# Kernel tuning notes

Measured on AMD Instinct MI355X. Metric: run time of the kernel, lower is better.

Reference implementation:

```python
import jax, jax.numpy as jnp
import numpy as np

# ---- problem constants (match init_kwargs / input_specs) ----
N = 10000        # atoms
E = 160000       # edges
G = 16           # graphs in batch
Z = 10           # num_elements
K = 64           # channels (count of 0e in hidden_irreps)
NB = 8           # num_bessel
SH = 9           # (max_ell+1)^2, max_ell=2
HID = 16         # MLP_irreps 16x0e
R_MAX = 5.0
AVG_NEI = 16.0
P = 5            # num_polynomial_cutoff
L_SLICES = ((0, 1, 0), (1, 4, 1), (4, 9, 2))  # (start, end, l) per irrep block


def _sph(u):
    # real spherical harmonics, 'component' normalization, lmax=2 -> 9 comps
    x, y, z = u[:, 0], u[:, 1], u[:, 2]
    s3, s15, s5 = 3.0 ** 0.5, 15.0 ** 0.5, 5.0 ** 0.5
    one = jnp.ones_like(x)
    return jnp.stack([one,
                      s3 * x, s3 * y, s3 * z,
                      s15 * x * y, s15 * y * z,
                      0.5 * s5 * (3.0 * z * z - 1.0),
                      s15 * x * z, 0.5 * s15 * (x * x - y * y)], axis=-1)


def _radial(r):
    # Bessel basis * polynomial cutoff (p=5)
    n = jnp.arange(1, NB + 1, dtype=r.dtype)
    bess = (2.0 / R_MAX) ** 0.5 * jnp.sin(n[None, :] * jnp.pi * r[:, None] / R_MAX) / r[:, None]
    xx = r / R_MAX
    f = (1.0 - 0.5 * (P + 1) * (P + 2) * xx ** P + P * (P + 2) * xx ** (P + 1)
         - 0.5 * P * (P + 1) * xx ** (P + 2)) * (xx < 1.0)
    return bess * f[:, None]


def _total_energy(positions, node_attrs, shifts, atomic_energies, W_embed, W_up,
                  R1, R2, R3, R4, W_out, W_sc, theta, W_mix, w_read0, Wr1, Wr2,
                  edge_index, batch):
    sender, receiver = edge_index[0], edge_index[1]
    vec = positions[receiver] - positions[sender] + shifts          # [E,3]
    r = jnp.sqrt(jnp.sum(vec * vec, axis=-1) + 1e-9)                # [E]
    u = vec / r[:, None]
    sh = _sph(u)                                                     # [E,9]
    edge_feats = _radial(r)                                          # [E,NB]

    node_e0 = node_attrs @ atomic_energies                           # [N]
    energies = jax.ops.segment_sum(node_e0, batch, num_segments=G)   # [G]

    feats = node_attrs @ W_embed                                     # [N,K] scalar feats
    for i in range(2):
        h = feats @ W_up[i]                                          # [N,K]
        xw = jax.nn.silu(edge_feats @ R1[i])
        xw = jax.nn.silu(xw @ R2[i])
        xw = jax.nn.silu(xw @ R3[i])
        rw = xw @ R4[i]                                              # [E,K] TP weights
        # channel-wise tensor product message + scatter to receiver
        m = rw[:, :, None] * h[sender][:, :, None] * sh[:, None, :]  # [E,K,9]
        A = jax.ops.segment_sum(m, receiver, num_segments=N) / AVG_NEI  # [N,K,9]
        A = jnp.concatenate([jnp.einsum('nkc,kj->njc', A[:, :, s:e], W_out[i, l])
                             for (s, e, l) in L_SLICES], axis=-1)    # per-l linear
        sc = jnp.einsum('nk,nz,zkj->nj', feats, node_attrs, W_sc[i])  # residual (0e)
        # symmetric-contraction product block (correlation=3), element-dependent
        a0 = A[:, :, 0]
        w = jnp.einsum('nz,pzk->pnk', node_attrs, theta[i])           # [3,N,K]
        B = (w[0] + w[1] * a0 + w[2] * a0 * a0)[:, :, None] * A      # [N,K,9]
        B = jnp.einsum('nkc,kj->njc', B, W_mix[i])
        B = B.at[:, :, 0].add(sc)
        feats = B[:, :, 0]                                            # invariant part
        if i == 0:
            node_e = feats @ w_read0                                  # linear readout
        else:
            node_e = jax.nn.silu(feats @ Wr1) @ Wr2                   # nonlinear readout
        energies = energies + jax.ops.segment_sum(node_e, batch, num_segments=G)
    return energies                                                   # [G]


def setup_inputs() -> dict:
    key = jax.random.key(0)
    ks = jax.random.split(key, 24)
    positions = jax.random.normal(ks[0], (N, 3), jnp.float32) * 1.5
    elems = jax.random.randint(ks[1], (N,), 0, Z)
    node_attrs = jax.nn.one_hot(elems, Z, dtype=jnp.float32)
    edge_index = jax.random.randint(ks[2], (2, E), 0, N)
    batch = jnp.sort(jax.random.randint(ks[3], (N,), 0, G))
    shifts = jnp.zeros((E, 3), jnp.float32)
    rn = lambda k, sh, s: jax.random.normal(k, sh, jnp.float32) * s
    return {
        'positions': positions, 'node_attrs': node_attrs, 'shifts': shifts,
        'atomic_energies': rn(ks[4], (Z,), 1.0),
        'W_embed': rn(ks[5], (Z, K), Z ** -0.5),
        'W_up': rn(ks[6], (2, K, K), K ** -0.5),
        'R1': rn(ks[7], (2, NB, 64), NB ** -0.5),
        'R2': rn(ks[8], (2, 64, 64), 64 ** -0.5),
        'R3': rn(ks[9], (2, 64, 64), 64 ** -0.5),
        'R4': rn(ks[10], (2, 64, K), 64 ** -0.5),
        'W_out': rn(ks[11], (2, 3, K, K), K ** -0.5),
        'W_sc': rn(ks[12], (2, Z, K, K), (Z * K) ** -0.5),
        'theta': rn(ks[13], (2, 3, Z, K), 0.1),
        'W_mix': rn(ks[14], (2, K, K), K ** -0.5),
        'w_read0': rn(ks[15], (K,), K ** -0.5),
        'Wr1': rn(ks[16], (K, HID), K ** -0.5),
        'Wr2': rn(ks[17], (HID,), HID ** -0.5),
        'edge_index': edge_index, 'batch': batch,
    }


def reference(positions, node_attrs, shifts, atomic_energies, W_embed, W_up,
              R1, R2, R3, R4, W_out, W_sc, theta, W_mix, w_read0, Wr1, Wr2,
              edge_index, batch):
    def energy(pos):
        return _total_energy(pos, node_attrs, shifts, atomic_energies, W_embed, W_up,
                             R1, R2, R3, R4, W_out, W_sc, theta, W_mix,
                             w_read0, Wr1, Wr2, edge_index, batch)
    total_energy, vjp_fn = jax.vjp(energy, positions)
    (g_pos,) = vjp_fn(jnp.ones((G,), positions.dtype))
    forces = -g_pos
    return total_energy, forces
```

## Files before the change

### kernel.cpp

```cpp
#include <hip/hip_runtime.h>
#include <math.h>

#define N_NODES 10000
#define N_EDGES 160000
#define G_SEG 16
#define ZDIM 10
#define KDIM 64
#define NBESS 8
#define HIDR 16
#define RMAXF 5.0f
#define AVG_NEI_F 16.0f
#define TBINS 256
#define ZROW (TBINS+1)

__device__ __forceinline__ float siluf(float x){ float s = 1.0f/(1.0f+expf(-x)); return x*s; }
__device__ __forceinline__ float dsiluf(float x){ float s = 1.0f/(1.0f+expf(-x)); return s*(1.0f + x*(1.0f-s)); }

__device__ __forceinline__ float waveReduce(float v){
  for (int off = 32; off > 0; off >>= 1) v += __shfl_down(v, off);
  return v;
}

#define GATHER_NODE(NODE, PTR, PACK, IDXEXPR, LOADH, OUT) { \
  int beg_ = PTR[NODE]; int deg_ = PTR[(NODE)+1] - beg_; \
  float a0_=0.f,a1_=0.f,a2_=0.f,a3_=0.f; \
  for (int base_=0; base_<deg_; base_+=64){ \
    int m_ = min(64, deg_-base_); \
    int b_l = ZROW; float f_l = 0.f; int ix_l = 0; \
    if (lane < m_){ \
      int4 pk = PACK[beg_+base_+lane]; \
      float tp_ = __int_as_float(pk.x) * (TBINS/RMAXF); \
      b_l = (int)tp_; f_l = tp_ - (float)b_l; ix_l = IDXEXPR; \
    } \
    int mr_ = (m_ + 7) & ~7; \
    for (int i_=0; i_<mr_; i_+=8){ \
      int b0_=__shfl(b_l,i_),   b1_=__shfl(b_l,i_+1), b2_=__shfl(b_l,i_+2), b3_=__shfl(b_l,i_+3); \
      int b4_=__shfl(b_l,i_+4), b5_=__shfl(b_l,i_+5), b6_=__shfl(b_l,i_+6), b7_=__shfl(b_l,i_+7); \
      float f0_=__shfl(f_l,i_),   f1_=__shfl(f_l,i_+1), f2_=__shfl(f_l,i_+2), f3_=__shfl(f_l,i_+3); \
      float f4_=__shfl(f_l,i_+4), f5_=__shfl(f_l,i_+5), f6_=__shfl(f_l,i_+6), f7_=__shfl(f_l,i_+7); \
      int s0_=__shfl(ix_l,i_),   s1_=__shfl(ix_l,i_+1), s2_=__shfl(ix_l,i_+2), s3_=__shfl(ix_l,i_+3); \
      int s4_=__shfl(ix_l,i_+4), s5_=__shfl(ix_l,i_+5), s6_=__shfl(ix_l,i_+6), s7_=__shfl(ix_l,i_+7); \
      float2 F0_=Ft2[b0_*KDIM+lane]; float h0_=LOADH(s0_); \
      float2 F1_=Ft2[b1_*KDIM+lane]; float h1_=LOADH(s1_); \
      float2 F2_=Ft2[b2_*KDIM+lane]; float h2_=LOADH(s2_); \
      float2 F3_=Ft2[b3_*KDIM+lane]; float h3_=LOADH(s3_); \
      float2 F4_=Ft2[b4_*KDIM+lane]; float h4_=LOADH(s4_); \
      float2 F5_=Ft2[b5_*KDIM+lane]; float h5_=LOADH(s5_); \
      float2 F6_=Ft2[b6_*KDIM+lane]; float h6_=LOADH(s6_); \
      float2 F7_=Ft2[b7_*KDIM+lane]; float h7_=LOADH(s7_); \
      a0_ += (F0_.x + f0_*(F0_.y-F0_.x))*h0_; a1_ += (F1_.x + f1_*(F1_.y-F1_.x))*h1_; \
      a2_ += (F2_.x + f2_*(F2_.y-F2_.x))*h2_; a3_ += (F3_.x + f3_*(F3_.y-F3_.x))*h3_; \
      a0_ += (F4_.x + f4_*(F4_.y-F4_.x))*h4_; a1_ += (F5_.x + f5_*(F5_.y-F5_.x))*h5_; \
      a2_ += (F6_.x + f6_*(F6_.y-F6_.x))*h6_; a3_ += (F7_.x + f7_*(F7_.y-F7_.x))*h7_; \
    } } \
  OUT = ((a0_+a1_)+(a2_+a3_)); }

#define COOPMV(INV, W, OUTV) { \
  lds_in[w][lane] = INV; \
  __syncthreads(); \
  { float p0_=0.f,p1_=0.f,p2_=0.f,p3__=0.f; \
    const float* Wb_ = (W) + (w*16)*KDIM + lane; \
    _Pragma("unroll") \
    for (int kk_=0; kk_<16; kk_++){ \
      float wrow_ = Wb_[kk_*KDIM]; \
      int k_ = w*16 + kk_; \
      p0_  += lds_in[0][k_]*wrow_; \
      p1_  += lds_in[1][k_]*wrow_; \
      p2_  += lds_in[2][k_]*wrow_; \
      p3__ += lds_in[3][k_]*wrow_; \
    } \
    lds_part[w][0][lane]=p0_; lds_part[w][1][lane]=p1_; \
    lds_part[w][2][lane]=p2_; lds_part[w][3][lane]=p3__; } \
  __syncthreads(); \
  OUTV = ((lds_part[0][w][lane]+lds_part[1][w][lane]) + \
          (lds_part[2][w][lane]+lds_part[3][w][lane])); }

#define MV4R(V, W, OUT) { \
  float x0_=0.f,x1_=0.f,x2_=0.f,x3_=0.f; \
  for (int k_=0;k_<KDIM;k_+=4){ \
    x0_ += __shfl(V,k_)  *W[k_*KDIM+lane]; \
    x1_ += __shfl(V,k_+1)*W[(k_+1)*KDIM+lane]; \
    x2_ += __shfl(V,k_+2)*W[(k_+2)*KDIM+lane]; \
    x3_ += __shfl(V,k_+3)*W[(k_+3)*KDIM+lane]; \
  } OUT = (x0_+x1_)+(x2_+x3_); }

#define LOADH_PLAIN(S) rows[(S)*KDIM + lane]
#define LOADH_G2(S)    gAr2c[(S)*KDIM + lane].x

#define NTABW 514
#define SETUP_BASE 153
#define NSETUP (SETUP_BASE + (NTABW+3)/4)

__global__ __launch_bounds__(256) void k_setup(
    const float* We, const float* Wup, const float* Wsc,
    const float* Wout, const float* Wmix,
    const float* Wr1,
    const float* attrs, const float* aE,
    const float* R1g, const float* R2g, const float* R3g, const float* R4g,
    float* M0, float* Msc0,
    float* WoT0, float* WoT1, float* WmixT0, float* WupT1,
    float* P1, float* Qtab,
    float2* Ft2_0, float2* Ft2_1, float* dF4f,
    int* z_buf, float* e_node){
  int blk = blockIdx.x, tid = threadIdx.x;
  const float* Wmix1 = Wmix + KDIM*KDIM;
  const float* Wsc1  = Wsc + ZDIM*KDIM*KDIM;
  if (blk < 5){
    int idx = blk*256 + tid;
    if (idx < 1280){
      int which = idx >= 640;
      int t = which ? idx - 640 : idx;
      int z = t >> 6, j = t & 63;
      float acc = 0.f;
      if (!which){
        #pragma unroll 8
        for (int k = 0; k < KDIM; k++) acc += We[z*KDIM + k] * Wup[k*KDIM + j];
        M0[z*KDIM + j] = acc;
      } else {
        #pragma unroll 8
        for (int k = 0; k < KDIM; k++) acc += We[z*KDIM + k] * Wsc[(z*KDIM + k)*KDIM + j];
        Msc0[z*KDIM + j] = acc;
      }
    }
  } else if (blk < 69){
    int t = (blk-5)*256 + tid;
    int arr = t >> 12;
    int rem = t & 4095;
    int j = rem >> 6, k = rem & 63;
    float v; float* dst;
    switch(arr){
      case 0: v = Wout[k*KDIM + j];                 dst = WoT0;   break;
      case 1: v = Wout[3*KDIM*KDIM + k*KDIM + j];   dst = WoT1;   break;
      case 2: v = Wmix[k*KDIM + j];                 dst = WmixT0; break;
      default:v = Wup[KDIM*KDIM + k*KDIM + j];      dst = WupT1;  break;
    }
    dst[rem] = v;
  } else if (blk < 73){
    int t = (blk-69)*256 + tid;
    int h = t >> 6, k = t & 63;
    float acc = 0.f;
    #pragma unroll 8
    for (int j = 0; j < KDIM; j++) acc += Wr1[j*HIDR + h] * Wmix1[k*KDIM + j];
    P1[h*KDIM + k] = acc;
  } else if (blk < 113){
    int t = (blk-73)*256 + tid;
    int z = t >> 10;
    int rem = t & 1023;
    int h = rem >> 6, k = rem & 63;
    float acc = 0.f;
    #pragma unroll 8
    for (int j = 0; j < KDIM; j++) acc += Wr1[j*HIDR + h] * Wsc1[(z*KDIM + k)*KDIM + j];
    Qtab[(z*HIDR + h)*KDIM + k] = acc;
  } else if (blk < SETUP_BASE){
    int n = (blk-113)*256 + tid;
    if (n < N_NODES){
      int z = 0;
      for (int i = 1; i < ZDIM; i++) if (attrs[n*ZDIM+i] > 0.5f) z = i;
      z_buf[n] = z;
      e_node[n] = aE[z];
    }
  } else {
    int w = tid >> 6, j = tid & 63;
    int wave_id = (blk - SETUP_BASE)*4 + w;
    if (wave_id >= NTABW) return;
    int i = wave_id / (TBINS+1);
    int t = wave_id % (TBINS+1);
    float efv = 0.f, defv = 0.f;
    {
      double r = (double)t * (double)RMAXF / (double)TBINS;
      double wfr = (double)(j+1) * M_PI / (double)RMAXF;
      double c = sqrt(2.0 / (double)RMAXF);
      double bess, dbess;
      if (r < 1e-12){ bess = c*wfr; dbess = 0.0; }
      else {
        double sw = sin(wfr*r), cw = cos(wfr*r);
        bess = c*sw/r;
        dbess = c*(wfr*cw*r - sw)/(r*r);
      }
      double xx = r / (double)RMAXF;
      double f = 0.0, df = 0.0;
      if (xx < 1.0){
        double x2 = xx*xx, x4 = x2*x2, x5 = x4*xx, x6 = x5*xx, x7 = x6*xx;
        f = 1.0 - 21.0*x5 + 35.0*x6 - 15.0*x7;
        df = (-105.0*x4 + 210.0*x5 - 105.0*x6) / (double)RMAXF;
      }
      efv  = (float)(bess*f);
      defv = (float)(dbess*f + bess*df);
    }
    const float* R1 = R1g + i*NBESS*KDIM;
    const float* R2 = R2g + i*KDIM*KDIM;
    const float* R3 = R3g + i*KDIM*KDIM;
    const float* R4 = R4g + i*KDIM*KDIM;
    float z = 0.f, dz = 0.f;
    #pragma unroll
    for (int b = 0; b < NBESS; b++){
      float ef = __shfl(efv, b), def = __shfl(defv, b);
      float wv = R1[b*KDIM+j];
      z += ef*wv; dz += def*wv;
    }
    float v = siluf(z), dv = dsiluf(z)*dz;
    z = 0.f; dz = 0.f;
    for (int k = 0; k < KDIM; k++){
      float xv = __shfl(v, k), dxv = __shfl(dv, k);
      float wv = R2[k*KDIM+j];
      z += xv*wv; dz += dxv*wv;
    }
    float v2 = siluf(z), dv2 = dsiluf(z)*dz;
    z = 0.f; dz = 0.f;
    for (int k = 0; k < KDIM; k++){
      float xv = __shfl(v2, k), dxv = __shfl(dv2, k);
      float wv = R3[k*KDIM+j];
      z += xv*wv; dz += dxv*wv;
    }
    float v3 = siluf(z), dv3 = dsiluf(z)*dz;
    z = 0.f; dz = 0.f;
    for (int k = 0; k < KDIM; k++){
      float xv = __shfl(v3, k), dxv = __shfl(dv3, k);
      float wv = R4[k*KDIM+j];
      z += xv*wv; dz += dxv*wv;
    }
    float2* Ft = i ? Ft2_1 : Ft2_0;
    Ft[t*KDIM+j].x = z;  if (t > 0) Ft[(t-1)*KDIM+j].y = z;
    dF4f[(t*KDIM+j)*4 + 2*i] = dz;
    if (t > 0) dF4f[((t-1)*KDIM+j)*4 + 2*i + 1] = dz;
    if (t == 0) Ft[ZROW*KDIM + j] = make_float2(0.f, 0.f);
  }
}

__global__ __launch_bounds__(256) void k_edge_setup(const float* pos, const float* shifts, const int* ei,
                                                    const int* z_buf,
                                                    float4* evec, int4* emeta,
                                                    int* cnt_r, int* cnt_s){
  int e = blockIdx.x*256 + threadIdx.x;
  int s = ei[e], rcv = ei[N_EDGES + e];
  float dx = pos[rcv*3+0] - pos[s*3+0] + shifts[e*3+0];
  float dy = pos[rcv*3+1] - pos[s*3+1] + shifts[e*3+1];
  float dz = pos[rcv*3+2] - pos[s*3+2] + shifts[e*3+2];
  float r = sqrtf(dx*dx + dy*dy + dz*dz + 1e-9f);
  evec[e] = make_float4(dx, dy, dz, r);
  emeta[e] = make_int4(__float_as_int(r), s, rcv, z_buf[s]);
  if (r < RMAXF){
    atomicAdd(&cnt_s[s], 1);
    atomicAdd(&cnt_r[rcv], 1);
  }
}

__global__ __launch_bounds__(1024) void k_scan(const int* cnt_r, int* ptr_r, int* cur_r,
                                               const int* cnt_s, int* ptr_s, int* cur_s){
  __shared__ int wtot[16];
  __shared__ int woff[16];
  int tid = threadIdx.x;
  int w = tid >> 6, lane = tid & 63;
  const int* cnt = blockIdx.x ? cnt_s : cnt_r;
  int* ptr = blockIdx.x ? ptr_s : ptr_r;
  int* cur = blockIdx.x ? cur_s : cur_r;
  const int per = 10;
  int start = tid*per;
  int csum = 0;
  int cl[per];
  #pragma unroll
  for (int t = 0; t < per; t++){
    int i = start + t;
    int c = (i < N_NODES) ? cnt[i] : 0;
    cl[t] = c; csum += c;
  }
  int v = csum;
  #pragma unroll
  for (int off = 1; off < 64; off <<= 1){
    int u = __shfl_up(v, off);
    if (lane >= off) v += u;
  }
  if (lane == 63) wtot[w] = v;
  __syncthreads();
  if (w == 0 && lane < 16){
    int t = wtot[lane];
    int sv = t;
    #pragma unroll
    for (int off = 1; off < 16; off <<= 1){
      int u = __shfl_up(sv, off);
      if (lane >= off) sv += u;
    }
    woff[lane] = sv - t;
    if (lane == 15) ptr[N_NODES] = sv;
  }
  __syncthreads();
  int run = woff[w] + v - csum;
  #pragma unroll
  for (int t = 0; t < per; t++){
    int i = start + t;
    if (i < N_NODES){ ptr[i] = run; cur[i] = run; run += cl[t]; }
  }
}

__global__ __launch_bounds__(256) void k_fill(const int4* emeta, int* cur_r, int* cur_s,
                                              int4* pr_pack, int4* ps_pack){
  int e = blockIdx.x*256 + threadIdx.x;
  int4 m = emeta[e];
  float r = __int_as_float(m.x);
  if (r >= RMAXF) return;
  int p = atomicAdd(&cur_s[m.y], 1);
  ps_pack[p] = make_int4(m.x, m.z, e, 0);
  int p2 = atomicAdd(&cur_r[m.z], 1);
  pr_pack[p2] = make_int4(m.x, m.y, m.w, e);
}

__global__ __launch_bounds__(256) void k_layer0_fwd(
    const int* z_buf, const int* ptr_r, const int4* pr_pack,
    const float2* Ft2, const float* M0,
    const float* Wout0, const float* theta0, const float* Wmix0,
    const float* Msc0, const float* w_read0,
    const float* Wup1, const float* Wsc1,
    float* A0_out, float* h1, float* sc1, float* e_node){
  __shared__ float lds_in[4][KDIM];
  __shared__ float lds_part[4][4][KDIM];
  int tid = threadIdx.x;
  int w = tid >> 6, lane = tid & 63;
  int node = blockIdx.x*4 + w;
  int z = z_buf[node];
  const float* rows = M0;
  float acc;
  GATHER_NODE(node, ptr_r, pr_pack, pk.z, LOADH_PLAIN, acc)
  acc *= (1.0f/AVG_NEI_F);
  float a0;
  COOPMV(acc, Wout0, a0)
  A0_out[node*KDIM+lane] = a0;
  float t0 = theta0[(0*ZDIM+z)*KDIM+lane];
  float t1 = theta0[(1*ZDIM+z)*KDIM+lane];
  float t2 = theta0[(2*ZDIM+z)*KDIM+lane];
  float v = (t0 + t1*a0 + t2*a0*a0)*a0;
  float f;
  COOPMV(v, Wmix0, f)
  f += Msc0[z*KDIM+lane];
  float p = waveReduce(f * w_read0[lane]);
  if (lane == 0) e_node[node] += p;
  float h;
  COOPMV(f, Wup1, h)
  h1[node*KDIM+lane] = h;
  const float* Wz = Wsc1 + z*KDIM*KDIM;
  float s;
  MV4R(f, Wz, s)
  sc1[node*KDIM+lane] = s;
}

__global__ __launch_bounds__(256) void k_layer1_fwd_bwd(
    const int* z_buf, const int* ptr_r, const int4* pr_pack,
    const float2* Ft2, const float* h1,
    const float* Wout1, const float* theta1, const float* Wmix1,
    const float* sc1, const float* Wr1, const float* Wr2,
    const float* P1, const float* Qtab, const float* WoT1, const float* w_read0,
    float2* gAr2, float* gF1, float* e_node){
  __shared__ float lds_in[4][KDIM];
  __shared__ float lds_part[4][4][KDIM];
  int tid = threadIdx.x;
  int w = tid >> 6, lane = tid & 63;
  int node = blockIdx.x*4 + w;
  int z = z_buf[node];
  const float* rows = h1;
  float acc;
  GATHER_NODE(node, ptr_r, pr_pack, pk.y, LOADH_PLAIN, acc)
  acc *= (1.0f/AVG_NEI_F);
  float a0;
  COOPMV(acc, Wout1, a0)
  float t0 = theta1[(0*ZDIM+z)*KDIM+lane];
  float t1 = theta1[(1*ZDIM+z)*KDIM+lane];
  float t2 = theta1[(2*ZDIM+z)*KDIM+lane];
  float v = (t0 + t1*a0 + t2*a0*a0)*a0;
  float f;
  COOPMV(v, Wmix1, f)
  f += sc1[node*KDIM+lane];
  int hh = lane & 15;
  float tp0 = 0.f, tp1 = 0.f;
  for (int j = 0; j < KDIM; j += 2){
    tp0 += __shfl(f,j)  *Wr1[j*HIDR+hh];
    tp1 += __shfl(f,j+1)*Wr1[(j+1)*HIDR+hh];
  }
  float tpart = tp0 + tp1;
  float wr2 = Wr2[hh];
  float ne = waveReduce(siluf(tpart)*wr2);
  if (lane == 0) e_node[node] += 0.25f*ne;
  float coeff = dsiluf(tpart)*wr2;
  float gP0=0.f, gP1=0.f, gs0=0.f, gs1=0.f;
  const float* Qz = Qtab + z*HIDR*KDIM;
  #pragma unroll
  for (int h2 = 0; h2 < HIDR; h2 += 2){
    float c0 = __shfl(coeff, h2), c1 = __shfl(coeff, h2+1);
    gP0 += c0*P1[h2*KDIM+lane];
    gP1 += c1*P1[(h2+1)*KDIM+lane];
    gs0 += c0*Qz[h2*KDIM+lane];
    gs1 += c1*Qz[(h2+1)*KDIM+lane];
  }
  gF1[node*KDIM+lane] = w_read0[lane] + gs0 + gs1;
  float u = t0 + 2.f*t1*a0 + 3.f*t2*a0*a0;
  float vl = (gP0+gP1)*u;
  float gAr;
  COOPMV(vl, WoT1, gAr)
  gAr2[node*KDIM+lane].x = gAr * (1.0f/AVG_NEI_F);
}

__global__ __launch_bounds__(256) void k_energy(const float* e_node, const int* batch, float* out_e){
  __shared__ float part[G_SEG];
  int tid = threadIdx.x;
  if (tid < G_SEG) part[tid] = 0.f;
  __syncthreads();
  int n = blockIdx.x*256 + tid;
  if (n < N_NODES) atomicAdd(&part[batch[n]], e_node[n]);
  __syncthreads();
  if (tid < G_SEG) atomicAdd(&out_e[tid], part[tid]);
}

__global__ __launch_bounds__(256) void k_bwd_gH0(
    const int* z_buf, const int* ptr_s, const int4* ps_pack,
    const float2* Ft2, const float2* gAr2c, const float* WupT1, const float* gF1,
    const float* A00, const float* WmixT0, const float* WoT0, const float* theta0,
    float2* gAr2){
  __shared__ float lds_in[4][KDIM];
  __shared__ float lds_part[4][4][KDIM];
  int tid = threadIdx.x;
  int w = tid >> 6, lane = tid & 63;
  int node = blockIdx.x*4 + w;
  float ga;
  GATHER_NODE(node, ptr_s, ps_pack, pk.y, LOADH_G2, ga)
  float gfh;
  COOPMV(ga, WupT1, gfh)
  float gt = gF1[node*KDIM+lane] + gfh;
  float gP;
  COOPMV(gt, WmixT0, gP)
  int z = z_buf[node];
  float a = A00[node*KDIM+lane];
  float t0 = theta0[(0*ZDIM+z)*KDIM+lane];
  float t1 = theta0[(1*ZDIM+z)*KDIM+lane];
  float t2 = theta0[(2*ZDIM+z)*KDIM+lane];
  float u = t0 + 2.f*t1*a + 3.f*t2*a*a;
  float vl = gP*u;
  float gAr;
  COOPMV(vl, WoT0, gAr)
  gAr2[node*KDIM+lane].y = gAr * (1.0f/AVG_NEI_F);
}

__global__ __launch_bounds__(256) void k_gr(const int4* emeta, const float4* dF4,
                                            const float2* gAr2, const float* h1, const float* M0,
                                            float4* evec){
  int tid = threadIdx.x;
  int w = tid>>6, lane = tid&63;
  int e = blockIdx.x*4 + w;
  int4 m = emeta[e];
  float r = __int_as_float(m.x);
  if (r >= RMAXF) return;
  float tp = r * (TBINS / RMAXF);
  int b = (int)tp; if (b > TBINS-1) b = TBINS-1;
  float fr = tp - (float)b;
  float4 d4 = dF4[b*KDIM + lane];
  float2 g  = gAr2[m.z*KDIM + lane];
  float hv1 = h1[m.y*KDIM + lane];
  float hv0 = M0[m.w*KDIM + lane];
  float v = g.x*hv1*(d4.z + fr*(d4.w - d4.z)) + g.y*hv0*(d4.x + fr*(d4.y - d4.x));
  v = waveReduce(v);
  if (lane == 0) evec[e].w = v / r;
}

__global__ __launch_bounds__(256) void k_force(const int* ptr_r, const int4* pr_pack,
                                               const int* ptr_s, const int4* ps_pack,
                                               const float4* evec,
                                               float* out_f){
  int tid = threadIdx.x;
  int node = blockIdx.x*16 + (tid >> 4);
  int li = tid & 15;
  float fx=0.f, fy=0.f, fz=0.f;
  int beg = ptr_r[node], end = ptr_r[node+1];
  for (int idx = beg + li; idx < end; idx += 16){
    int e = pr_pack[idx].w;
    float4 ev = evec[e];
    fx -= ev.w*ev.x; fy -= ev.w*ev.y; fz -= ev.w*ev.z;
  }
  beg = ptr_s[node]; end = ptr_s[node+1];
  for (int idx = beg + li; idx < end; idx += 16){
    int e = ps_pack[idx].z;
    float4 ev = evec[e];
    fx += ev.w*ev.x; fy += ev.w*ev.y; fz += ev.w*ev.z;
  }
  #pragma unroll
  for (int off = 8; off > 0; off >>= 1){
    fx += __shfl_xor(fx, off);
    fy += __shfl_xor(fy, off);
    fz += __shfl_xor(fz, off);
  }
  if (li == 0){
    out_f[node*3+0] = fx; out_f[node*3+1] = fy; out_f[node*3+2] = fz;
  }
}

extern "C" void kernel_launch(void* const* d_in, const int* in_sizes, int n_in,
                              void* d_out, int out_size, void* d_ws, size_t ws_size,
                              hipStream_t stream){
  const float* pos    = (const float*)d_in[0];
  const float* attrs  = (const float*)d_in[1];
  const float* shifts = (const float*)d_in[2];
  const float* aE     = (const float*)d_in[3];
  const float* We     = (const float*)d_in[4];
  const float* Wup    = (const float*)d_in[5];
  const float* R1     = (const float*)d_in[6];
  const float* R2     = (const float*)d_in[7];
  const float* R3     = (const float*)d_in[8];
  const float* R4     = (const float*)d_in[9];
  const float* Wout   = (const float*)d_in[10];
  const float* Wsc    = (const float*)d_in[11];
  const float* theta  = (const float*)d_in[12];
  const float* Wmix   = (const float*)d_in[13];
  const float* w_read0= (const float*)d_in[14];
  const float* Wr1    = (const float*)d_in[15];
  const float* Wr2    = (const float*)d_in[16];
  const int*   ei     = (const int*)d_in[17];
  const int*   batch  = (const int*)d_in[18];

  char* base = (char*)d_ws;
  size_t off = 0;
  auto alloc = [&](size_t bytes)->void*{
    void* p = base + off;
    off = (off + bytes + 255) & ~(size_t)255;
    return p;
  };
  float4* evec   = (float4*)alloc(N_EDGES*sizeof(float4));
  int4*   emeta  = (int4*)alloc(N_EDGES*sizeof(int4));
  int4*   pr_pack= (int4*)alloc(N_EDGES*sizeof(int4));
  int4*   ps_pack= (int4*)alloc(N_EDGES*sizeof(int4));
  float*  e_node = (float*)alloc(N_NODES*sizeof(float));
  float*  h1     = (float*)alloc(N_NODES*KDIM*sizeof(float));
  float*  sc1    = (float*)alloc(N_NODES*KDIM*sizeof(float));
  float*  A00    = (float*)alloc(N_NODES*KDIM*sizeof(float));
  float*  gF1    = (float*)alloc(N_NODES*KDIM*sizeof(float));
  float2* gAr2   = (float2*)alloc(N_NODES*KDIM*sizeof(float2));
  float2* Ft2_0  = (float2*)alloc((TBINS+2)*KDIM*sizeof(float2));
  float2* Ft2_1  = (float2*)alloc((TBINS+2)*KDIM*sizeof(float2));
  float4* dF4    = (float4*)alloc((TBINS+1)*KDIM*sizeof(float4));
  float*  M0     = (float*)alloc(ZDIM*KDIM*sizeof(float));
  float*  Msc0   = (float*)alloc(ZDIM*KDIM*sizeof(float));
  float*  WoT0   = (float*)alloc(KDIM*KDIM*sizeof(float));
  float*  WoT1   = (float*)alloc(KDIM*KDIM*sizeof(float));
  float*  WmixT0 = (float*)alloc(KDIM*KDIM*sizeof(float));
  float*  WupT1  = (float*)alloc(KDIM*KDIM*sizeof(float));
  float*  P1     = (float*)alloc(HIDR*KDIM*sizeof(float));
  float*  Qtab   = (float*)alloc(ZDIM*HIDR*KDIM*sizeof(float));
  int* z_buf = (int*)alloc(N_NODES*sizeof(int));
  int* cnt_r = (int*)alloc(N_NODES*sizeof(int));
  int* cnt_s = (int*)alloc(N_NODES*sizeof(int));
  int* ptr_r = (int*)alloc((N_NODES+1)*sizeof(int));
  int* ptr_s = (int*)alloc((N_NODES+1)*sizeof(int));
  int* cur_r = (int*)alloc(N_NODES*sizeof(int));
  int* cur_s = (int*)alloc(N_NODES*sizeof(int));

  float* out_e = (float*)d_out;
  float* out_f = out_e + G_SEG;

  hipMemsetAsync(d_out, 0, (size_t)out_size*sizeof(float), stream);
  hipMemsetAsync(cnt_r, 0, N_NODES*sizeof(int), stream);
  hipMemsetAsync(cnt_s, 0, N_NODES*sizeof(int), stream);

  const int NB4 = N_NODES/4;
  const int EB  = N_EDGES/256;
  const int EB4 = N_EDGES/4;
  const int NBt = (N_NODES+255)/256;

  const float* Wup1 = Wup + KDIM*KDIM;
  const float* Wsc1 = Wsc + ZDIM*KDIM*KDIM;
  const float* Wout1 = Wout + 3*KDIM*KDIM;
  const float* theta1 = theta + 3*ZDIM*KDIM;
  const float* Wmix1 = Wmix + KDIM*KDIM;

  k_setup<<<NSETUP,256,0,stream>>>(We, Wup, Wsc, Wout, Wmix, Wr1, attrs, aE,
                                   R1, R2, R3, R4,
                                   M0, Msc0, WoT0, WoT1, WmixT0, WupT1, P1, Qtab,
                                   Ft2_0, Ft2_1, (float*)dF4,
                                   z_buf, e_node);
  k_edge_setup<<<EB,256,0,stream>>>(pos, shifts, ei, z_buf, evec, emeta, cnt_r, cnt_s);
  k_scan<<<2,1024,0,stream>>>(cnt_r, ptr_r, cur_r, cnt_s, ptr_s, cur_s);
  k_fill<<<EB,256,0,stream>>>(emeta, cur_r, cur_s, pr_pack, ps_pack);

  k_layer0_fwd<<<NB4,256,0,stream>>>(z_buf, ptr_r, pr_pack, Ft2_0, M0,
      Wout, theta, Wmix, Msc0, w_read0, Wup1, Wsc1,
      A00, h1, sc1, e_node);
  k_layer1_fwd_bwd<<<NB4,256,0,stream>>>(z_buf, ptr_r, pr_pack, Ft2_1, h1,
      Wout1, theta1, Wmix1, sc1, Wr1, Wr2,
      P1, Qtab, WoT1, w_read0,
      gAr2, gF1, e_node);
  k_energy<<<NBt,256,0,stream>>>(e_node, batch, out_e);

  k_bwd_gH0<<<NB4,256,0,stream>>>(z_buf, ptr_s, ps_pack, Ft2_1, gAr2, WupT1, gF1,
      A00, WmixT0, WoT0, theta, gAr2);
  k_gr<<<EB4,256,0,stream>>>(emeta, dF4, gAr2, h1, M0, evec);
  k_force<<<N_NODES/16,256,0,stream>>>(ptr_r, pr_pack, ptr_s, ps_pack, evec, out_f);
}
```

Before: 262.6 us.

## Transpose weight tables, use readlane matvecs, fuse energy reduction, repack k_gr

Precomputes transposed copies of Wsc1, Wr1, P1 and Qtab so per-lane matvecs read contiguous float4 rows with wave-uniform readlane broadcasts instead of shuffles. COOPMV now reads LDS inputs as float4. The separate k_energy kernel is removed, and per-node energies are atomically added to the graph totals inside the layer-1 kernel. k_gr is remapped from one wave per edge to 16 lanes per edge with float4 loads and a 16-lane xor reduction. In exchange, k_setup gets more blocks, and the per-node atomics on only 16 outputs may contend.

```diff
diff --git a/kernel.cpp b/kernel.cpp
--- a/kernel.cpp
+++ b/kernel.cpp
@@ -19,6 +19,10 @@
 __device__ __forceinline__ float waveReduce(float v){
   for (int off = 32; off > 0; off >>= 1) v += __shfl_down(v, off);
   return v;
+}
+
+__device__ __forceinline__ float rlane(float v, int l){
+  return __int_as_float(__builtin_amdgcn_readlane(__float_as_int(v), l));
 }
 
 #define GATHER_NODE(NODE, PTR, PACK, IDXEXPR, LOADH, OUT) { \
@@ -61,13 +65,19 @@
   { float p0_=0.f,p1_=0.f,p2_=0.f,p3__=0.f; \
     const float* Wb_ = (W) + (w*16)*KDIM + lane; \
     _Pragma("unroll") \
-    for (int kk_=0; kk_<16; kk_++){ \
-      float wrow_ = Wb_[kk_*KDIM]; \
-      int k_ = w*16 + kk_; \
-      p0_  += lds_in[0][k_]*wrow_; \
-      p1_  += lds_in[1][k_]*wrow_; \
-      p2_  += lds_in[2][k_]*wrow_; \
-      p3__ += lds_in[3][k_]*wrow_; \
+    for (int kq_=0; kq_<4; kq_++){ \
+      float4 x0_ = *(const float4*)&lds_in[0][w*16+4*kq_]; \
+      float4 x1_ = *(const float4*)&lds_in[1][w*16+4*kq_]; \
+      float4 x2_ = *(const float4*)&lds_in[2][w*16+4*kq_]; \
+      float4 x3_ = *(const float4*)&lds_in[3][w*16+4*kq_]; \
+      float w0_ = Wb_[(4*kq_+0)*KDIM]; \
+      float w1_ = Wb_[(4*kq_+1)*KDIM]; \
+      float w2_ = Wb_[(4*kq_+2)*KDIM]; \
+      float w3_ = Wb_[(4*kq_+3)*KDIM]; \
+      p0_  += x0_.x*w0_ + x0_.y*w1_ + x0_.z*w2_ + x0_.w*w3_; \
+      p1_  += x1_.x*w0_ + x1_.y*w1_ + x1_.z*w2_ + x1_.w*w3_; \
+      p2_  += x2_.x*w0_ + x2_.y*w1_ + x2_.z*w2_ + x2_.w*w3_; \
+      p3__ += x3_.x*w0_ + x3_.y*w1_ + x3_.z*w2_ + x3_.w*w3_; \
     } \
     lds_part[w][0][lane]=p0_; lds_part[w][1][lane]=p1_; \
     lds_part[w][2][lane]=p2_; lds_part[w][3][lane]=p3__; } \
@@ -75,20 +85,25 @@
   OUTV = ((lds_part[0][w][lane]+lds_part[1][w][lane]) + \
           (lds_part[2][w][lane]+lds_part[3][w][lane])); }
 
-#define MV4R(V, W, OUT) { \
-  float x0_=0.f,x1_=0.f,x2_=0.f,x3_=0.f; \
-  for (int k_=0;k_<KDIM;k_+=4){ \
-    x0_ += __shfl(V,k_)  *W[k_*KDIM+lane]; \
-    x1_ += __shfl(V,k_+1)*W[(k_+1)*KDIM+lane]; \
-    x2_ += __shfl(V,k_+2)*W[(k_+2)*KDIM+lane]; \
-    x3_ += __shfl(V,k_+3)*W[(k_+3)*KDIM+lane]; \
-  } OUT = (x0_+x1_)+(x2_+x3_); }
+#define MVTROW(XV, MT, ROW, OUT) { \
+  const float4* Mr_ = (const float4*)((MT) + (ROW)*KDIM); \
+  float m0a_=0.f,m1a_=0.f,m2a_=0.f,m3a_=0.f; \
+  _Pragma("unroll") \
+  for (int kq_=0; kq_<KDIM/4; kq_++){ \
+    float4 mm_ = Mr_[kq_]; \
+    m0a_ += rlane(XV,4*kq_+0)*mm_.x; \
+    m1a_ += rlane(XV,4*kq_+1)*mm_.y; \
+    m2a_ += rlane(XV,4*kq_+2)*mm_.z; \
+    m3a_ += rlane(XV,4*kq_+3)*mm_.w; \
+  } \
+  OUT = (m0a_+m1a_)+(m2a_+m3a_); }
+#define MVT(XV, MT, OUT) MVTROW(XV, MT, lane, OUT)
 
 #define LOADH_PLAIN(S) rows[(S)*KDIM + lane]
 #define LOADH_G2(S)    gAr2c[(S)*KDIM + lane].x
 
 #define NTABW 514
-#define SETUP_BASE 153
+#define SETUP_BASE 317
 #define NSETUP (SETUP_BASE + (NTABW+3)/4)
 
 __global__ __launch_bounds__(256) void k_setup(
@@ -99,7 +114,7 @@
     const float* R1g, const float* R2g, const float* R3g, const float* R4g,
     float* M0, float* Msc0,
     float* WoT0, float* WoT1, float* WmixT0, float* WupT1,
-    float* P1, float* Qtab,
+    float* P1T, float* QtabT, float* WscT1, float* Wr1T,
     float2* Ft2_0, float2* Ft2_1, float* dF4f,
     int* z_buf, float* e_node){
   int blk = blockIdx.x, tid = threadIdx.x;
@@ -141,7 +156,7 @@
     float acc = 0.f;
     #pragma unroll 8
     for (int j = 0; j < KDIM; j++) acc += Wr1[j*HIDR + h] * Wmix1[k*KDIM + j];
-    P1[h*KDIM + k] = acc;
+    P1T[k*HIDR + h] = acc;
   } else if (blk < 113){
     int t = (blk-73)*256 + tid;
     int z = t >> 10;
@@ -150,8 +165,8 @@
     float acc = 0.f;
     #pragma unroll 8
     for (int j = 0; j < KDIM; j++) acc += Wr1[j*HIDR + h] * Wsc1[(z*KDIM + k)*KDIM + j];
-    Qtab[(z*HIDR + h)*KDIM + k] = acc;
-  } else if (blk < SETUP_BASE){
+    QtabT[(z*KDIM + k)*HIDR + h] = acc;
+  } else if (blk < 153){
     int n = (blk-113)*256 + tid;
     if (n < N_NODES){
       int z = 0;
@@ -159,6 +174,15 @@
       z_buf[n] = z;
       e_node[n] = aE[z];
     }
+  } else if (blk < 313){
+    int t = (blk-153)*256 + tid;
+    int zz = t >> 12; int rem = t & 4095;
+    int j = rem >> 6, k = rem & 63;
+    WscT1[(zz*KDIM + j)*KDIM + k] = Wsc1[(zz*KDIM + k)*KDIM + j];
+  } else if (blk < SETUP_BASE){
+    int t = (blk-313)*256 + tid;
+    int h = t >> 6, j = t & 63;
+    Wr1T[h*KDIM + j] = Wr1[j*HIDR + h];
   } else {
     int w = tid >> 6, j = tid & 63;
     int wave_id = (blk - SETUP_BASE)*4 + w;
@@ -309,9 +333,9 @@
     const float2* Ft2, const float* M0,
     const float* Wout0, const float* theta0, const float* Wmix0,
     const float* Msc0, const float* w_read0,
-    const float* Wup1, const float* Wsc1,
+    const float* Wup1, const float* WscT1,
     float* A0_out, float* h1, float* sc1, float* e_node){
-  __shared__ float lds_in[4][KDIM];
+  __shared__ __align__(16) float lds_in[4][KDIM];
   __shared__ float lds_part[4][4][KDIM];
   int tid = threadIdx.x;
   int w = tid >> 6, lane = tid & 63;
@@ -336,26 +360,26 @@
   float h;
   COOPMV(f, Wup1, h)
   h1[node*KDIM+lane] = h;
-  const float* Wz = Wsc1 + z*KDIM*KDIM;
   float s;
-  MV4R(f, Wz, s)
+  MVT(f, WscT1 + z*KDIM*KDIM, s)
   sc1[node*KDIM+lane] = s;
 }
 
 __global__ __launch_bounds__(256) void k_layer1_fwd_bwd(
     const int* z_buf, const int* ptr_r, const int4* pr_pack,
-    const float2* Ft2, const float* h1,
+    const float2* Ft2, const float* h1rows,
     const float* Wout1, const float* theta1, const float* Wmix1,
-    const float* sc1, const float* Wr1, const float* Wr2,
-    const float* P1, const float* Qtab, const float* WoT1, const float* w_read0,
-    float2* gAr2, float* gF1, float* e_node){
-  __shared__ float lds_in[4][KDIM];
+    const float* sc1, const float* Wr1T, const float* Wr2,
+    const float* P1T, const float* QtabT, const float* WoT1, const float* w_read0,
+    const float* e_node, const int* batch,
+    float2* gAr2, float* gF1, float* out_e){
+  __shared__ __align__(16) float lds_in[4][KDIM];
   __shared__ float lds_part[4][4][KDIM];
   int tid = threadIdx.x;
   int w = tid >> 6, lane = tid & 63;
   int node = blockIdx.x*4 + w;
   int z = z_buf[node];
-  const float* rows = h1;
+  const float* rows = h1rows;
   float acc;
   GATHER_NODE(node, ptr_r, pr_pack, pk.y, LOADH_PLAIN, acc)
   acc *= (1.0f/AVG_NEI_F);
@@ -369,43 +393,32 @@
   COOPMV(v, Wmix1, f)
   f += sc1[node*KDIM+lane];
   int hh = lane & 15;
-  float tp0 = 0.f, tp1 = 0.f;
-  for (int j = 0; j < KDIM; j += 2){
-    tp0 += __shfl(f,j)  *Wr1[j*HIDR+hh];
-    tp1 += __shfl(f,j+1)*Wr1[(j+1)*HIDR+hh];
-  }
-  float tpart = tp0 + tp1;
+  float tpart;
+  MVTROW(f, Wr1T, hh, tpart)
   float wr2 = Wr2[hh];
   float ne = waveReduce(siluf(tpart)*wr2);
-  if (lane == 0) e_node[node] += 0.25f*ne;
+  if (lane == 0) atomicAdd(&out_e[batch[node]], e_node[node] + 0.25f*ne);
   float coeff = dsiluf(tpart)*wr2;
-  float gP0=0.f, gP1=0.f, gs0=0.f, gs1=0.f;
-  const float* Qz = Qtab + z*HIDR*KDIM;
-  #pragma unroll
-  for (int h2 = 0; h2 < HIDR; h2 += 2){
-    float c0 = __shfl(coeff, h2), c1 = __shfl(coeff, h2+1);
-    gP0 += c0*P1[h2*KDIM+lane];
-    gP1 += c1*P1[(h2+1)*KDIM+lane];
-    gs0 += c0*Qz[h2*KDIM+lane];
-    gs1 += c1*Qz[(h2+1)*KDIM+lane];
-  }
-  gF1[node*KDIM+lane] = w_read0[lane] + gs0 + gs1;
+  float gP, gs;
+  { const float4* Pp_ = (const float4*)(P1T + lane*HIDR);
+    const float4* Qp_ = (const float4*)(QtabT + (z*KDIM + lane)*HIDR);
+    float pa0_=0.f,pa1_=0.f,pa2_=0.f,pa3_=0.f, qa0_=0.f,qa1_=0.f,qa2_=0.f,qa3_=0.f;
+    #pragma unroll
+    for (int hq_=0; hq_<HIDR/4; hq_++){
+      float4 pm_ = Pp_[hq_]; float4 qm_ = Qp_[hq_];
+      float c0_=rlane(coeff,4*hq_+0), c1_=rlane(coeff,4*hq_+1);
+      float c2_=rlane(coeff,4*hq_+2), c3_=rlane(coeff,4*hq_+3);
+      pa0_ += c0_*pm_.x; pa1_ += c1_*pm_.y; pa2_ += c2_*pm_.z; pa3_ += c3_*pm_.w;
+      qa0_ += c0_*qm_.x; qa1_ += c1_*qm_.y; qa2_ += c2_*qm_.z; qa3_ += c3_*qm_.w;
+    }
+    gP = (pa0_+pa1_)+(pa2_+pa3_); gs = (qa0_+qa1_)+(qa2_+qa3_);
+  }
+  gF1[node*KDIM+lane] = w_read0[lane] + gs;
   float u = t0 + 2.f*t1*a0 + 3.f*t2*a0*a0;
-  float vl = (gP0+gP1)*u;
+  float vl = gP*u;
   float gAr;
   COOPMV(vl, WoT1, gAr)
   gAr2[node*KDIM+lane].x = gAr * (1.0f/AVG_NEI_F);
-}
-
-__global__ __launch_bounds__(256) void k_energy(const float* e_node, const int* batch, float* out_e){
-  __shared__ float part[G_SEG];
-  int tid = threadIdx.x;
-  if (tid < G_SEG) part[tid] = 0.f;
-  __syncthreads();
-  int n = blockIdx.x*256 + tid;
-  if (n < N_NODES) atomicAdd(&part[batch[n]], e_node[n]);
-  __syncthreads();
-  if (tid < G_SEG) atomicAdd(&out_e[tid], part[tid]);
 }
 
 __global__ __launch_bounds__(256) void k_bwd_gH0(
@@ -413,7 +426,7 @@
     const float2* Ft2, const float2* gAr2c, const float* WupT1, const float* gF1,
     const float* A00, const float* WmixT0, const float* WoT0, const float* theta0,
     float2* gAr2){
-  __shared__ float lds_in[4][KDIM];
+  __shared__ __align__(16) float lds_in[4][KDIM];
   __shared__ float lds_part[4][4][KDIM];
   int tid = threadIdx.x;
   int w = tid >> 6, lane = tid & 63;
@@ -441,21 +454,29 @@
                                             const float2* gAr2, const float* h1, const float* M0,
                                             float4* evec){
   int tid = threadIdx.x;
-  int w = tid>>6, lane = tid&63;
-  int e = blockIdx.x*4 + w;
+  int e = blockIdx.x*16 + (tid >> 4);
+  int li = tid & 15;
   int4 m = emeta[e];
   float r = __int_as_float(m.x);
   if (r >= RMAXF) return;
   float tp = r * (TBINS / RMAXF);
   int b = (int)tp; if (b > TBINS-1) b = TBINS-1;
   float fr = tp - (float)b;
-  float4 d4 = dF4[b*KDIM + lane];
-  float2 g  = gAr2[m.z*KDIM + lane];
-  float hv1 = h1[m.y*KDIM + lane];
-  float hv0 = M0[m.w*KDIM + lane];
-  float v = g.x*hv1*(d4.z + fr*(d4.w - d4.z)) + g.y*hv0*(d4.x + fr*(d4.y - d4.x));
-  v = waveReduce(v);
-  if (lane == 0) evec[e].w = v / r;
+  int k0 = li*4;
+  const float4* dp = dF4 + b*KDIM + k0;
+  float4 d0 = dp[0], d1 = dp[1], d2 = dp[2], d3 = dp[3];
+  const float4* gp = (const float4*)(gAr2 + m.z*KDIM + k0);
+  float4 g01 = gp[0], g23 = gp[1];
+  float4 hv = *(const float4*)(h1 + m.y*KDIM + k0);
+  float4 mv = *(const float4*)(M0 + m.w*KDIM + k0);
+  float v;
+  v  = g01.x*hv.x*(d0.z + fr*(d0.w-d0.z)) + g01.y*mv.x*(d0.x + fr*(d0.y-d0.x));
+  v += g01.z*hv.y*(d1.z + fr*(d1.w-d1.z)) + g01.w*mv.y*(d1.x + fr*(d1.y-d1.x));
+  v += g23.x*hv.z*(d2.z + fr*(d2.w-d2.z)) + g23.y*mv.z*(d2.x + fr*(d2.y-d2.x));
+  v += g23.z*hv.w*(d3.z + fr*(d3.w-d3.z)) + g23.w*mv.w*(d3.x + fr*(d3.y-d3.x));
+  #pragma unroll
+  for (int off = 8; off > 0; off >>= 1) v += __shfl_xor(v, off);
+  if (li == 0) evec[e].w = v / r;
 }
 
 __global__ __launch_bounds__(256) void k_force(const int* ptr_r, const int4* pr_pack,
@@ -538,8 +559,10 @@
   float*  WoT1   = (float*)alloc(KDIM*KDIM*sizeof(float));
   float*  WmixT0 = (float*)alloc(KDIM*KDIM*sizeof(float));
   float*  WupT1  = (float*)alloc(KDIM*KDIM*sizeof(float));
-  float*  P1     = (float*)alloc(HIDR*KDIM*sizeof(float));
-  float*  Qtab   = (float*)alloc(ZDIM*HIDR*KDIM*sizeof(float));
+  float*  P1T    = (float*)alloc(KDIM*HIDR*sizeof(float));
+  float*  QtabT  = (float*)alloc(ZDIM*KDIM*HIDR*sizeof(float));
+  float*  WscT1  = (float*)alloc(ZDIM*KDIM*KDIM*sizeof(float));
+  float*  Wr1T   = (float*)alloc(HIDR*KDIM*sizeof(float));
   int* z_buf = (int*)alloc(N_NODES*sizeof(int));
   int* cnt_r = (int*)alloc(N_NODES*sizeof(int));
   int* cnt_s = (int*)alloc(N_NODES*sizeof(int));
@@ -557,18 +580,16 @@
 
   const int NB4 = N_NODES/4;
   const int EB  = N_EDGES/256;
-  const int EB4 = N_EDGES/4;
-  const int NBt = (N_NODES+255)/256;
 
   const float* Wup1 = Wup + KDIM*KDIM;
-  const float* Wsc1 = Wsc + ZDIM*KDIM*KDIM;
   const float* Wout1 = Wout + 3*KDIM*KDIM;
   const float* theta1 = theta + 3*ZDIM*KDIM;
   const float* Wmix1 = Wmix + KDIM*KDIM;
 
   k_setup<<<NSETUP,256,0,stream>>>(We, Wup, Wsc, Wout, Wmix, Wr1, attrs, aE,
                                    R1, R2, R3, R4,
-                                   M0, Msc0, WoT0, WoT1, WmixT0, WupT1, P1, Qtab,
+                                   M0, Msc0, WoT0, WoT1, WmixT0, WupT1,
+                                   P1T, QtabT, WscT1, Wr1T,
                                    Ft2_0, Ft2_1, (float*)dF4,
                                    z_buf, e_node);
   k_edge_setup<<<EB,256,0,stream>>>(pos, shifts, ei, z_buf, evec, emeta, cnt_r, cnt_s);
@@ -576,16 +597,15 @@
   k_fill<<<EB,256,0,stream>>>(emeta, cur_r, cur_s, pr_pack, ps_pack);
 
   k_layer0_fwd<<<NB4,256,0,stream>>>(z_buf, ptr_r, pr_pack, Ft2_0, M0,
-      Wout, theta, Wmix, Msc0, w_read0, Wup1, Wsc1,
+      Wout, theta, Wmix, Msc0, w_read0, Wup1, WscT1,
       A00, h1, sc1, e_node);
   k_layer1_fwd_bwd<<<NB4,256,0,stream>>>(z_buf, ptr_r, pr_pack, Ft2_1, h1,
-      Wout1, theta1, Wmix1, sc1, Wr1, Wr2,
-      P1, Qtab, WoT1, w_read0,
-      gAr2, gF1, e_node);
-  k_energy<<<NBt,256,0,stream>>>(e_node, batch, out_e);
+      Wout1, theta1, Wmix1, sc1, Wr1T, Wr2,
+      P1T, QtabT, WoT1, w_read0, e_node, batch,
+      gAr2, gF1, out_e);
 
   k_bwd_gH0<<<NB4,256,0,stream>>>(z_buf, ptr_s, ps_pack, Ft2_1, gAr2, WupT1, gF1,
       A00, WmixT0, WoT0, theta, gAr2);
-  k_gr<<<EB4,256,0,stream>>>(emeta, dF4, gAr2, h1, M0, evec);
+  k_gr<<<N_EDGES/16,256,0,stream>>>(emeta, dF4, gAr2, h1, M0, evec);
   k_force<<<N_NODES/16,256,0,stream>>>(ptr_r, pr_pack, ptr_s, ps_pack, evec, out_f);
 }
```

Measured after the change: 368.3 us. +40.3%, slower.
